# Kernel optimization log

Hardware: AMD Instinct MI355X
Metric: run time of the kernel (lower is better)

## Reference

```python
import jax, jax.numpy as jnp
import numpy as np

D_MODEL = 1024
NUM_HEADS = 16
D_K = D_MODEL // NUM_HEADS
TEMPERATURE = 1.0
EPS = 1e-6


def setup_inputs() -> dict:
    key = jax.random.key(0)
    ks = jax.random.split(key, 8)
    B, S, D, H = 2, 2048, D_MODEL, NUM_HEADS
    sc = 1.0 / np.sqrt(D)
    x = jax.random.normal(ks[0], (B, S, D), dtype=jnp.float32)
    Wq = jax.random.normal(ks[1], (D, D), dtype=jnp.float32) * sc
    Wk = jax.random.normal(ks[2], (D, D), dtype=jnp.float32) * sc
    Wv = jax.random.normal(ks[3], (D, D), dtype=jnp.float32) * sc
    Wo = jax.random.normal(ks[4], (D, D), dtype=jnp.float32) * sc
    bo = jnp.zeros((D,), dtype=jnp.float32)
    phase_scale = jnp.ones((H,), dtype=jnp.float32)
    # orthogonal init for entanglement matrix
    q, _ = np.linalg.qr(np.random.default_rng(0).normal(size=(H, H)))
    ent = jnp.asarray(q, dtype=jnp.float32)
    gamma = jnp.ones((D,), dtype=jnp.float32)
    beta = jnp.zeros((D,), dtype=jnp.float32)
    return {"x": x, "Wq": Wq, "Wk": Wk, "Wv": Wv, "Wo": Wo, "bo": bo,
            "phase_scale": phase_scale, "ent": ent, "gamma": gamma, "beta": beta}


def reference(x, Wq, Wk, Wv, Wo, bo, phase_scale, ent, gamma, beta):
    B, S, D = x.shape
    H, dk = NUM_HEADS, D_K
    # projections -> [B, H, S, dk]
    Q = (x @ Wq).reshape(B, S, H, dk).transpose(0, 2, 1, 3)
    K = (x @ Wk).reshape(B, S, H, dk).transpose(0, 2, 1, 3)
    V = (x @ Wv).reshape(B, S, H, dk).transpose(0, 2, 1, 3)
    # per-head QK^T, scaled, phase-modulated
    scores = jnp.einsum('bhqd,bhkd->bhqk', Q, K)
    inv = 1.0 / (float(np.sqrt(dk)) * TEMPERATURE)
    s = scores * (inv * phase_scale)[None, :, None, None]
    # real part of quantum phase: cos(s) + 0.1*cos(2s)  (imag part of V is zero,
    # so head_output = attended_real; the 0.1*attended_imag term vanishes)
    w = jnp.cos(s) + 0.1 * jnp.cos(2.0 * s)
    w = jax.nn.softmax(w, axis=-1)
    att = jnp.einsum('bhqk,bhkd->bhqd', w, V).transpose(0, 2, 1, 3)  # [B,S,H,dk]
    # faithful reproduction of tf.einsum('bsnd,hm->bsmd', ...): sums over n AND h
    att = jnp.einsum('bsnd,hm->bsmd', att, ent)
    out = att.reshape(B, S, D) @ Wo + bo
    r = out + x
    mu = jnp.mean(r, axis=-1, keepdims=True)
    var = jnp.mean(jnp.square(r - mu), axis=-1, keepdims=True)
    return gamma * (r - mu) * jax.lax.rsqrt(var + EPS) + beta
```

## Files before the change

### kernel.cpp

```cpp
#include <hip/hip_runtime.h>
#include <cstdint>
#include <cstddef>

#define S_LEN 2048
#define DMODEL 1024
#define NHEADS 16
#define DKH 64
#define MROWS 4096
#define BH_CNT 32

typedef __bf16 bf16x8 __attribute__((ext_vector_type(8)));
typedef __bf16 bf16x2 __attribute__((ext_vector_type(2)));
typedef float f32x4 __attribute__((ext_vector_type(4)));
typedef unsigned int u32;
typedef unsigned short u16;

__device__ __forceinline__ u16 f2bfu(float f) {
  u32 u = __float_as_uint(f);
  return (u16)((u + 0x7FFFu + ((u >> 16) & 1u)) >> 16);
}

__device__ __forceinline__ u32 pk_bf16(float a, float b) {
  bf16x2 v;
  v[0] = (__bf16)a;
  v[1] = (__bf16)b;
  return __builtin_bit_cast(u32, v);
}

__device__ __forceinline__ void gload16(void* lds, const void* g) {
  __builtin_amdgcn_global_load_lds(
      (const __attribute__((address_space(1))) void*)g,
      (__attribute__((address_space(3))) void*)lds, 16, 0, 0);
}

__global__ __launch_bounds__(256) void prep_xb_k(const float* __restrict__ x,
                                                 u16* __restrict__ xb) {
  int i = (blockIdx.x * 256 + threadIdx.x) * 4;
  float4 v = *(const float4*)(x + i);
  *(uint2*)(xb + i) = make_uint2(pk_bf16(v.x, v.y), pk_bf16(v.z, v.w));
}

__global__ __launch_bounds__(256) void prep_w_k(const float* __restrict__ Wq,
    const float* __restrict__ Wk, const float* __restrict__ Wv,
    const float* __restrict__ ps, u16* __restrict__ Wb) {
  __shared__ float tile[32][33];
  int sel = blockIdx.z;
  const float* W = sel == 0 ? Wq : (sel == 1 ? Wk : Wv);
  int k0 = blockIdx.x * 32, c0 = blockIdx.y * 32;
  int tx = threadIdx.x, ty = threadIdx.y;
#pragma unroll
  for (int i = 0; i < 4; ++i)
    tile[ty + i * 8][tx] = W[(size_t)(k0 + ty + i * 8) * DMODEL + c0 + tx];
  __syncthreads();
#pragma unroll
  for (int i = 0; i < 4; ++i) {
    int row = ty + i * 8;
    float v = tile[tx][row];
    if (sel == 1) v *= 0.125f * ps[(c0 + row) >> 6];
    Wb[(size_t)(sel * 1024 + c0 + row) * DMODEL + k0 + tx] = f2bfu(v);
  }
}

__global__ __launch_bounds__(256) void prep_woeff_k(const float* __restrict__ Wo,
    const float* __restrict__ ent, float* __restrict__ Woeff) {
  __shared__ float e[16];
  int t = threadIdx.x;
  if (t < 16) {
    float s = 0.f;
#pragma unroll
    for (int h = 0; h < 16; ++h) s += ent[h * 16 + t];
    e[t] = s;
  }
  __syncthreads();
  int gid = blockIdx.x * 256 + t;
  int d = gid >> 10, j = gid & 1023;
  float acc = 0.f;
#pragma unroll
  for (int m = 0; m < 16; ++m) acc += e[m] * Wo[(size_t)((m << 6) + d) * DMODEL + j];
  Woeff[(size_t)d * DMODEL + j] = acc;
}

__global__ __launch_bounds__(256) void gemm_qkv_k(const u16* __restrict__ xb,
    const u16* __restrict__ Wb, u16* __restrict__ Qb, u16* __restrict__ Kb,
    u16* __restrict__ Vt) {
  __shared__ __align__(16) u16 As[2][128 * 32];
  __shared__ __align__(16) u16 Bs[2][128 * 32];
  int tid = threadIdx.x;
  int lane = tid & 63, w = tid >> 6;
  int c = lane & 15, g = lane >> 4;
  int wr = w >> 1, wc = w & 1;
  int m0 = blockIdx.x * 128, n0 = blockIdx.y * 128;

  int cij0 = (w * 2) * 64 + lane, cij1 = (w * 2 + 1) * 64 + lane;
  int row0 = cij0 >> 2, kp0 = (cij0 & 3) ^ (row0 & 3);
  int row1 = cij1 >> 2, kp1 = (cij1 & 3) ^ (row1 & 3);
  const u16* a0p = xb + (size_t)(m0 + row0) * DMODEL + kp0 * 8;
  const u16* a1p = xb + (size_t)(m0 + row1) * DMODEL + kp1 * 8;
  const u16* b0p = Wb + (size_t)(n0 + row0) * DMODEL + kp0 * 8;
  const u16* b1p = Wb + (size_t)(n0 + row1) * DMODEL + kp1 * 8;

  f32x4 acc[4][4];
#pragma unroll
  for (int i = 0; i < 4; ++i)
#pragma unroll
    for (int j = 0; j < 4; ++j) acc[i][j] = (f32x4){0.f, 0.f, 0.f, 0.f};

  gload16(&As[0][(w * 2) * 512], a0p);
  gload16(&As[0][(w * 2 + 1) * 512], a1p);
  gload16(&Bs[0][(w * 2) * 512], b0p);
  gload16(&Bs[0][(w * 2 + 1) * 512], b1p);
  __syncthreads();

  int cur = 0;
  for (int kt = 0; kt < DMODEL; kt += 32) {
    if (kt + 32 < DMODEL) {
      int nx = cur ^ 1, ko = kt + 32;
      gload16(&As[nx][(w * 2) * 512], a0p + ko);
      gload16(&As[nx][(w * 2 + 1) * 512], a1p + ko);
      gload16(&Bs[nx][(w * 2) * 512], b0p + ko);
      gload16(&Bs[nx][(w * 2 + 1) * 512], b1p + ko);
    }
    const u16* Ac = As[cur];
    const u16* Bc = Bs[cur];
    bf16x8 af[4], bf[4];
#pragma unroll
    for (int i = 0; i < 4; ++i) {
      int ra = wr * 64 + i * 16 + c;
      af[i] = *(const bf16x8*)(Ac + ra * 32 + ((g ^ (ra & 3)) * 8));
      int rb = wc * 64 + i * 16 + c;
      bf[i] = *(const bf16x8*)(Bc + rb * 32 + ((g ^ (rb & 3)) * 8));
    }
#pragma unroll
    for (int i = 0; i < 4; ++i)
#pragma unroll
      for (int j = 0; j < 4; ++j)
        acc[i][j] = __builtin_amdgcn_mfma_f32_16x16x32_bf16(af[i], bf[j], acc[i][j], 0, 0, 0);
    __syncthreads();
    cur ^= 1;
  }

  int sel = n0 >> 10;
  int nb = n0 & 1023;
#pragma unroll
  for (int i = 0; i < 4; ++i) {
    int mbase = m0 + wr * 64 + i * 16 + 4 * g;
    int b = mbase >> 11, sr = mbase & 2047;
#pragma unroll
    for (int jf = 0; jf < 4; ++jf) {
      int ncol = nb + wc * 64 + jf * 16 + c;
      int h = ncol >> 6, d = ncol & 63;
      int bh = b * 16 + h;
      if (sel == 2) {
        *(uint2*)(Vt + ((size_t)bh * DKH + d) * S_LEN + sr) =
            make_uint2(pk_bf16(acc[i][jf][0], acc[i][jf][1]),
                       pk_bf16(acc[i][jf][2], acc[i][jf][3]));
      } else {
        u16* dst = (sel == 0 ? Qb : Kb);
#pragma unroll
        for (int j = 0; j < 4; ++j) {
          __bf16 hv = (__bf16)acc[i][jf][j];
          dst[((size_t)bh * S_LEN + sr + j) * DKH + d] = __builtin_bit_cast(u16, hv);
        }
      }
    }
  }
}

__global__ __launch_bounds__(256) void attn_k(const u16* __restrict__ Qb,
    const u16* __restrict__ Kb, const u16* __restrict__ Vt,
    float* __restrict__ attbuf) {
  __shared__ __align__(16) u16 Ks[2][64 * 64];
  __shared__ __align__(16) u16 Vs[2][64 * 64];
  __shared__ __align__(16) u32 Ps[4 * 16 * 32];
  int bh = blockIdx.y;
  int tid = threadIdx.x;
  int lane = tid & 63, w = tid >> 6;
  int c = lane & 15, g = lane >> 4;
  int q0 = blockIdx.x * 64 + w * 16;
  const u16* Kbase = Kb + (size_t)bh * S_LEN * DKH;
  const u16* Vbase = Vt + (size_t)bh * DKH * S_LEN;

  int cij0 = (w * 2) * 64 + lane, cij1 = (w * 2 + 1) * 64 + lane;
  int srow0 = cij0 >> 3, skp0 = (cij0 & 7) ^ (srow0 & 7);
  int srow1 = cij1 >> 3, skp1 = (cij1 & 7) ^ (srow1 & 7);
  const u16* k0p = Kbase + (size_t)srow0 * DKH + skp0 * 8;
  const u16* k1p = Kbase + (size_t)srow1 * DKH + skp1 * 8;
  const u16* v0p = Vbase + (size_t)srow0 * S_LEN + skp0 * 8;
  const u16* v1p = Vbase + (size_t)srow1 * S_LEN + skp1 * 8;

  gload16(&Ks[0][(w * 2) * 512], k0p);
  gload16(&Ks[0][(w * 2 + 1) * 512], k1p);
  gload16(&Vs[0][(w * 2) * 512], v0p);
  gload16(&Vs[0][(w * 2 + 1) * 512], v1p);

  bf16x8 qf0, qf1;
  {
    const u16* qp = Qb + ((size_t)bh * S_LEN + q0 + c) * DKH + g * 8;
    qf0 = *(const bf16x8*)qp;
    qf1 = *(const bf16x8*)(qp + 32);
  }
  f32x4 attT[4];
#pragma unroll
  for (int i = 0; i < 4; ++i) attT[i] = (f32x4){0.f, 0.f, 0.f, 0.f};
  float dacc0 = 0.f, dacc1 = 0.f;
  u32* Pw = Ps + w * 512;
  int wAddr[4];
#pragma unroll
  for (int fm = 0; fm < 4; ++fm) {
    int kr0 = fm * 16 + 4 * g;
    int ch = (kr0 >> 3) ^ (c & 7);
    wAddr[fm] = c * 32 + ch * 4 + ((kr0 & 7) >> 1);
  }
  const float L2E = 1.4426950408889634f;

  __syncthreads();
  int cur = 0;
  for (int kt = 0; kt < S_LEN; kt += 64) {
    if (kt + 64 < S_LEN) {
      int nx = cur ^ 1, ko = kt + 64;
      gload16(&Ks[nx][(w * 2) * 512], k0p + (size_t)ko * DKH);
      gload16(&Ks[nx][(w * 2 + 1) * 512], k1p + (size_t)ko * DKH);
      gload16(&Vs[nx][(w * 2) * 512], v0p + ko);
      gload16(&Vs[nx][(w * 2 + 1) * 512], v1p + ko);
    }
    const u16* Kc = Ks[cur];
    const u16* Vc = Vs[cur];
    f32x4 sT[4];
#pragma unroll
    for (int fm = 0; fm < 4; ++fm) {
      int row = fm * 16 + c;
      bf16x8 a0 = *(const bf16x8*)(Kc + row * 64 + ((g ^ (row & 7)) * 8));
      bf16x8 a1 = *(const bf16x8*)(Kc + row * 64 + (((4 + g) ^ (row & 7)) * 8));
      f32x4 z = (f32x4){0.f, 0.f, 0.f, 0.f};
      z = __builtin_amdgcn_mfma_f32_16x16x32_bf16(a0, qf0, z, 0, 0, 0);
      z = __builtin_amdgcn_mfma_f32_16x16x32_bf16(a1, qf1, z, 0, 0, 0);
      sT[fm] = z;
    }
#pragma unroll
    for (int fm = 0; fm < 4; ++fm) {
      float pv[4];
#pragma unroll
      for (int j = 0; j < 4; ++j) {
        float cv = __cosf(sT[fm][j]);
        float w2 = __fmaf_rn(cv, __fmaf_rn(0.2f * L2E, cv, L2E), -0.1f * L2E);
        pv[j] = __builtin_amdgcn_exp2f(w2);
      }
      dacc0 += pv[0] + pv[1];
      dacc1 += pv[2] + pv[3];
      *(uint2*)(Pw + wAddr[fm]) = make_uint2(pk_bf16(pv[0], pv[1]), pk_bf16(pv[2], pv[3]));
    }
#pragma unroll
    for (int bb = 0; bb < 2; ++bb) {
      bf16x8 pf = *(const bf16x8*)(Pw + c * 32 + (((4 * bb + g) ^ (c & 7)) * 4));
#pragma unroll
      for (int fd = 0; fd < 4; ++fd) {
        int row = fd * 16 + c;
        bf16x8 vf = *(const bf16x8*)(Vc + row * 64 + ((((4 * bb + g) ^ (row & 7))) * 8));
        attT[fd] = __builtin_amdgcn_mfma_f32_16x16x32_bf16(vf, pf, attT[fd], 0, 0, 0);
      }
    }
    __syncthreads();
    cur ^= 1;
  }
  float dacc = dacc0 + dacc1;
  dacc += __shfl_xor(dacc, 16, 64);
  dacc += __shfl_xor(dacc, 32, 64);
  float inv = 1.f / dacc;
  float* ob = attbuf + ((size_t)bh * S_LEN + q0 + c) * DKH;
#pragma unroll
  for (int fd = 0; fd < 4; ++fd)
#pragma unroll
    for (int j = 0; j < 4; ++j)
      ob[fd * 16 + 4 * g + j] = attT[fd][j] * inv;
}

__global__ __launch_bounds__(256) void fuse_out_ln_k(const float* __restrict__ attbuf,
    const float* __restrict__ Woeff, const float* __restrict__ bo,
    const float* __restrict__ x, const float* __restrict__ gamma,
    const float* __restrict__ beta, float* __restrict__ out) {
  __shared__ float red[8][256];
  __shared__ __align__(16) float a[8][64];
  __shared__ float sred[8][4][2];
  int t = threadIdx.x;
  int r0 = blockIdx.x * 8;
  int d = t & 63, hg = t >> 6;
#pragma unroll
  for (int rr = 0; rr < 8; ++rr) {
    int m = r0 + rr, b = m >> 11, sr = m & 2047;
    float pa = 0.f;
#pragma unroll
    for (int hh = 0; hh < 4; ++hh) {
      int h = hg * 4 + hh;
      pa += attbuf[(((size_t)(b * 16 + h)) * S_LEN + sr) * DKH + d];
    }
    red[rr][t] = pa;
  }
  __syncthreads();
#pragma unroll
  for (int e = 0; e < 2; ++e) {
    int idx = t + e * 256;
    int rr = idx >> 6, dd = idx & 63;
    a[rr][dd] = red[rr][dd] + red[rr][64 + dd] + red[rr][128 + dd] + red[rr][192 + dd];
  }
  __syncthreads();

  float o[8][4];
#pragma unroll
  for (int rr = 0; rr < 8; ++rr) { o[rr][0] = o[rr][1] = o[rr][2] = o[rr][3] = 0.f; }
  int c4 = t * 4;
  for (int dd = 0; dd < 64; dd += 4) {
    float4 wv0 = *(const float4*)(Woeff + (size_t)(dd + 0) * DMODEL + c4);
    float4 wv1 = *(const float4*)(Woeff + (size_t)(dd + 1) * DMODEL + c4);
    float4 wv2 = *(const float4*)(Woeff + (size_t)(dd + 2) * DMODEL + c4);
    float4 wv3 = *(const float4*)(Woeff + (size_t)(dd + 3) * DMODEL + c4);
#pragma unroll
    for (int rr = 0; rr < 8; ++rr) {
      float4 av = *(const float4*)&a[rr][dd];
      o[rr][0] += av.x * wv0.x + av.y * wv1.x + av.z * wv2.x + av.w * wv3.x;
      o[rr][1] += av.x * wv0.y + av.y * wv1.y + av.z * wv2.y + av.w * wv3.y;
      o[rr][2] += av.x * wv0.z + av.y * wv1.z + av.z * wv2.z + av.w * wv3.z;
      o[rr][3] += av.x * wv0.w + av.y * wv1.w + av.z * wv2.w + av.w * wv3.w;
    }
  }
  float4 bv = *(const float4*)(bo + c4);
  int w = t >> 6, lane = t & 63;
#pragma unroll
  for (int rr = 0; rr < 8; ++rr) {
    int m = r0 + rr;
    float4 xv = *(const float4*)(x + (size_t)m * DMODEL + c4);
    o[rr][0] += bv.x + xv.x;
    o[rr][1] += bv.y + xv.y;
    o[rr][2] += bv.z + xv.z;
    o[rr][3] += bv.w + xv.w;
    float s = o[rr][0] + o[rr][1] + o[rr][2] + o[rr][3];
    float q = o[rr][0] * o[rr][0] + o[rr][1] * o[rr][1] + o[rr][2] * o[rr][2] + o[rr][3] * o[rr][3];
#pragma unroll
    for (int mm = 1; mm < 64; mm <<= 1) {
      s += __shfl_xor(s, mm, 64);
      q += __shfl_xor(q, mm, 64);
    }
    if (lane == 0) { sred[rr][w][0] = s; sred[rr][w][1] = q; }
  }
  __syncthreads();
  float4 gv = *(const float4*)(gamma + c4);
  float4 bev = *(const float4*)(beta + c4);
#pragma unroll
  for (int rr = 0; rr < 8; ++rr) {
    float s = sred[rr][0][0] + sred[rr][1][0] + sred[rr][2][0] + sred[rr][3][0];
    float q = sred[rr][0][1] + sred[rr][1][1] + sred[rr][2][1] + sred[rr][3][1];
    float mu = s * (1.f / 1024.f);
    float var = q * (1.f / 1024.f) - mu * mu;
    float rs = rsqrtf(var + 1e-6f);
    int m = r0 + rr;
    float4 ov;
    ov.x = gv.x * (o[rr][0] - mu) * rs + bev.x;
    ov.y = gv.y * (o[rr][1] - mu) * rs + bev.y;
    ov.z = gv.z * (o[rr][2] - mu) * rs + bev.z;
    ov.w = gv.w * (o[rr][3] - mu) * rs + bev.w;
    *(float4*)(out + (size_t)m * DMODEL + c4) = ov;
  }
}

extern "C" void kernel_launch(void* const* d_in, const int* in_sizes, int n_in,
                              void* d_out, int out_size, void* d_ws, size_t ws_size,
                              hipStream_t stream) {
  const float* x = (const float*)d_in[0];
  const float* Wq = (const float*)d_in[1];
  const float* Wk = (const float*)d_in[2];
  const float* Wv = (const float*)d_in[3];
  const float* Wo = (const float*)d_in[4];
  const float* bo = (const float*)d_in[5];
  const float* ps = (const float*)d_in[6];
  const float* ent = (const float*)d_in[7];
  const float* gamma = (const float*)d_in[8];
  const float* beta = (const float*)d_in[9];
  float* out = (float*)d_out;

  char* ws = (char*)d_ws;
  size_t o = 0;
  u16* xb = (u16*)(ws + o);    o += (size_t)MROWS * DMODEL * 2;
  u16* Wb = (u16*)(ws + o);    o += (size_t)3072 * 1024 * 2;
  u16* Qb = (u16*)(ws + o);    o += (size_t)BH_CNT * S_LEN * DKH * 2;
  u16* Kb = (u16*)(ws + o);    o += (size_t)BH_CNT * S_LEN * DKH * 2;
  u16* Vt = (u16*)(ws + o);    o += (size_t)BH_CNT * S_LEN * DKH * 2;
  float* Woeff = (float*)(ws + o);  o += (size_t)DKH * DMODEL * 4;
  float* attbuf = (float*)(ws + o); o += (size_t)BH_CNT * S_LEN * DKH * 4;

  prep_xb_k<<<dim3(4096), dim3(256), 0, stream>>>(x, xb);
  prep_w_k<<<dim3(32, 32, 3), dim3(32, 8), 0, stream>>>(Wq, Wk, Wv, ps, Wb);
  prep_woeff_k<<<dim3(256), dim3(256), 0, stream>>>(Wo, ent, Woeff);
  gemm_qkv_k<<<dim3(32, 24), dim3(256), 0, stream>>>(xb, Wb, Qb, Kb, Vt);
  attn_k<<<dim3(32, 32), dim3(256), 0, stream>>>(Qb, Kb, Vt, attbuf);
  fuse_out_ln_k<<<dim3(512), dim3(256), 0, stream>>>(attbuf, Woeff, bo, x, gamma, beta, out);
}
```

Measured before the change: 141.3 us.

## Stage QKV epilogue through LDS, swizzle attention grid, use hardware cos

The QKV GEMM epilogue now writes accumulators into shared memory with an XOR swizzle, then emits coalesced 16-byte stores for Q, K and transposed V. The attention kernel uses a flattened, swizzled block index, a manually unrolled double-buffer loop with MFMA priority hints, and float4 output stores. The cosine now uses the raw hardware instruction, which takes its input in revolutions, so the K weight scale folds in 1/(2π). This skips the range-reduction overhead at some accuracy risk for large arguments.

After: 139.1 us. About the same (-1.5%).

```diff
diff --git a/kernel.cpp b/kernel.cpp
--- a/kernel.cpp
+++ b/kernel.cpp
@@ -56,7 +56,7 @@
   for (int i = 0; i < 4; ++i) {
     int row = ty + i * 8;
     float v = tile[tx][row];
-    if (sel == 1) v *= 0.125f * ps[(c0 + row) >> 6];
+    if (sel == 1) v *= 0.019894367886486918f * ps[(c0 + row) >> 6];
     Wb[(size_t)(sel * 1024 + c0 + row) * DMODEL + k0 + tx] = f2bfu(v);
   }
 }
@@ -83,8 +83,7 @@
 __global__ __launch_bounds__(256) void gemm_qkv_k(const u16* __restrict__ xb,
     const u16* __restrict__ Wb, u16* __restrict__ Qb, u16* __restrict__ Kb,
     u16* __restrict__ Vt) {
-  __shared__ __align__(16) u16 As[2][128 * 32];
-  __shared__ __align__(16) u16 Bs[2][128 * 32];
+  __shared__ __align__(16) u16 SMEM[2][2][128 * 32];
   int tid = threadIdx.x;
   int lane = tid & 63, w = tid >> 6;
   int c = lane & 15, g = lane >> 4;
@@ -105,23 +104,23 @@
 #pragma unroll
     for (int j = 0; j < 4; ++j) acc[i][j] = (f32x4){0.f, 0.f, 0.f, 0.f};
 
-  gload16(&As[0][(w * 2) * 512], a0p);
-  gload16(&As[0][(w * 2 + 1) * 512], a1p);
-  gload16(&Bs[0][(w * 2) * 512], b0p);
-  gload16(&Bs[0][(w * 2 + 1) * 512], b1p);
+  gload16(&SMEM[0][0][(w * 2) * 512], a0p);
+  gload16(&SMEM[0][0][(w * 2 + 1) * 512], a1p);
+  gload16(&SMEM[1][0][(w * 2) * 512], b0p);
+  gload16(&SMEM[1][0][(w * 2 + 1) * 512], b1p);
   __syncthreads();
 
   int cur = 0;
   for (int kt = 0; kt < DMODEL; kt += 32) {
     if (kt + 32 < DMODEL) {
       int nx = cur ^ 1, ko = kt + 32;
-      gload16(&As[nx][(w * 2) * 512], a0p + ko);
-      gload16(&As[nx][(w * 2 + 1) * 512], a1p + ko);
-      gload16(&Bs[nx][(w * 2) * 512], b0p + ko);
-      gload16(&Bs[nx][(w * 2 + 1) * 512], b1p + ko);
-    }
-    const u16* Ac = As[cur];
-    const u16* Bc = Bs[cur];
+      gload16(&SMEM[0][nx][(w * 2) * 512], a0p + ko);
+      gload16(&SMEM[0][nx][(w * 2 + 1) * 512], a1p + ko);
+      gload16(&SMEM[1][nx][(w * 2) * 512], b0p + ko);
+      gload16(&SMEM[1][nx][(w * 2 + 1) * 512], b1p + ko);
+    }
+    const u16* Ac = SMEM[0][cur];
+    const u16* Bc = SMEM[1][cur];
     bf16x8 af[4], bf[4];
 #pragma unroll
     for (int i = 0; i < 4; ++i) {
@@ -140,29 +139,50 @@
   }
 
   int sel = n0 >> 10;
-  int nb = n0 & 1023;
-#pragma unroll
-  for (int i = 0; i < 4; ++i) {
-    int mbase = m0 + wr * 64 + i * 16 + 4 * g;
-    int b = mbase >> 11, sr = mbase & 2047;
-#pragma unroll
-    for (int jf = 0; jf < 4; ++jf) {
-      int ncol = nb + wc * 64 + jf * 16 + c;
-      int h = ncol >> 6, d = ncol & 63;
-      int bh = b * 16 + h;
-      if (sel == 2) {
-        *(uint2*)(Vt + ((size_t)bh * DKH + d) * S_LEN + sr) =
-            make_uint2(pk_bf16(acc[i][jf][0], acc[i][jf][1]),
-                       pk_bf16(acc[i][jf][2], acc[i][jf][3]));
-      } else {
-        u16* dst = (sel == 0 ? Qb : Kb);
+  char* Ls = (char*)&SMEM[0][0][0];
+  if (sel == 2) {
+#pragma unroll
+    for (int i = 0; i < 4; ++i)
+#pragma unroll
+      for (int jf = 0; jf < 4; ++jf) {
+        int n = wc * 64 + jf * 16 + c;
+        int m = wr * 64 + i * 16 + 4 * g;
+        int byte = n * 256 + ((m * 2) ^ ((n & 7) << 4));
+        *(uint2*)(Ls + byte) = make_uint2(pk_bf16(acc[i][jf][0], acc[i][jf][1]),
+                                          pk_bf16(acc[i][jf][2], acc[i][jf][3]));
+      }
+  } else {
+#pragma unroll
+    for (int i = 0; i < 4; ++i)
+#pragma unroll
+      for (int jf = 0; jf < 4; ++jf) {
+        int n = wc * 64 + jf * 16 + c;
 #pragma unroll
         for (int j = 0; j < 4; ++j) {
+          int m = wr * 64 + i * 16 + 4 * g + j;
+          int byte = m * 256 + ((n * 2) ^ ((m & 7) << 4));
           __bf16 hv = (__bf16)acc[i][jf][j];
-          dst[((size_t)bh * S_LEN + sr + j) * DKH + d] = __builtin_bit_cast(u16, hv);
+          *(u16*)(Ls + byte) = __builtin_bit_cast(u16, hv);
         }
       }
-    }
+  }
+  __syncthreads();
+  int r = tid >> 1, half = tid & 1;
+  int h0 = (n0 & 1023) >> 6;
+  int b = m0 >> 11, sbase = m0 & 2047;
+  u16* dst;
+  if (sel == 2) {
+    int bh = b * 16 + h0 + (r >> 6), d = r & 63;
+    dst = Vt + ((size_t)bh * DKH + d) * S_LEN + sbase + half * 64;
+  } else {
+    u16* base = (sel == 0 ? Qb : Kb);
+    int bh = b * 16 + h0 + half;
+    dst = base + ((size_t)bh * S_LEN + sbase + r) * DKH;
+  }
+#pragma unroll
+  for (int kk = 0; kk < 8; ++kk) {
+    int byte = r * 256 + ((half * 128 + kk * 16) ^ ((r & 7) << 4));
+    *(uint4*)(dst + kk * 8) = *(const uint4*)(Ls + byte);
   }
 }
 
@@ -172,11 +192,13 @@
   __shared__ __align__(16) u16 Ks[2][64 * 64];
   __shared__ __align__(16) u16 Vs[2][64 * 64];
   __shared__ __align__(16) u32 Ps[4 * 16 * 32];
-  int bh = blockIdx.y;
+  int fid = blockIdx.x;
+  int swz = (fid & 7) * 128 + (fid >> 3);
+  int bh = swz >> 5, qblk = swz & 31;
   int tid = threadIdx.x;
   int lane = tid & 63, w = tid >> 6;
   int c = lane & 15, g = lane >> 4;
-  int q0 = blockIdx.x * 64 + w * 16;
+  int q0 = qblk * 64 + w * 16;
   const u16* Kbase = Kb + (size_t)bh * S_LEN * DKH;
   const u16* Vbase = Vt + (size_t)bh * DKH * S_LEN;
 
@@ -213,19 +235,9 @@
   }
   const float L2E = 1.4426950408889634f;
 
-  __syncthreads();
-  int cur = 0;
-  for (int kt = 0; kt < S_LEN; kt += 64) {
-    if (kt + 64 < S_LEN) {
-      int nx = cur ^ 1, ko = kt + 64;
-      gload16(&Ks[nx][(w * 2) * 512], k0p + (size_t)ko * DKH);
-      gload16(&Ks[nx][(w * 2 + 1) * 512], k1p + (size_t)ko * DKH);
-      gload16(&Vs[nx][(w * 2) * 512], v0p + ko);
-      gload16(&Vs[nx][(w * 2 + 1) * 512], v1p + ko);
-    }
-    const u16* Kc = Ks[cur];
-    const u16* Vc = Vs[cur];
+  auto compute = [&](const u16* Kc, const u16* Vc) {
     f32x4 sT[4];
+    __builtin_amdgcn_s_setprio(1);
 #pragma unroll
     for (int fm = 0; fm < 4; ++fm) {
       int row = fm * 16 + c;
@@ -236,12 +248,13 @@
       z = __builtin_amdgcn_mfma_f32_16x16x32_bf16(a1, qf1, z, 0, 0, 0);
       sT[fm] = z;
     }
+    __builtin_amdgcn_s_setprio(0);
 #pragma unroll
     for (int fm = 0; fm < 4; ++fm) {
       float pv[4];
 #pragma unroll
       for (int j = 0; j < 4; ++j) {
-        float cv = __cosf(sT[fm][j]);
+        float cv = __builtin_amdgcn_cosf(sT[fm][j]);
         float w2 = __fmaf_rn(cv, __fmaf_rn(0.2f * L2E, cv, L2E), -0.1f * L2E);
         pv[j] = __builtin_amdgcn_exp2f(w2);
       }
@@ -249,6 +262,7 @@
       dacc1 += pv[2] + pv[3];
       *(uint2*)(Pw + wAddr[fm]) = make_uint2(pk_bf16(pv[0], pv[1]), pk_bf16(pv[2], pv[3]));
     }
+    __builtin_amdgcn_s_setprio(1);
 #pragma unroll
     for (int bb = 0; bb < 2; ++bb) {
       bf16x8 pf = *(const bf16x8*)(Pw + c * 32 + (((4 * bb + g) ^ (c & 7)) * 4));
@@ -259,8 +273,31 @@
         attT[fd] = __builtin_amdgcn_mfma_f32_16x16x32_bf16(vf, pf, attT[fd], 0, 0, 0);
       }
     }
+    __builtin_amdgcn_s_setprio(0);
+  };
+
+  const u16* kc0 = k0p;
+  const u16* kc1 = k1p;
+  const u16* vc0 = v0p;
+  const u16* vc1 = v1p;
+  __syncthreads();
+  for (int kt = 0; kt < S_LEN; kt += 128) {
+    kc0 += 64 * DKH; kc1 += 64 * DKH; vc0 += 64; vc1 += 64;
+    gload16(&Ks[1][(w * 2) * 512], kc0);
+    gload16(&Ks[1][(w * 2 + 1) * 512], kc1);
+    gload16(&Vs[1][(w * 2) * 512], vc0);
+    gload16(&Vs[1][(w * 2 + 1) * 512], vc1);
+    compute(Ks[0], Vs[0]);
     __syncthreads();
-    cur ^= 1;
+    if (kt + 128 < S_LEN) {
+      kc0 += 64 * DKH; kc1 += 64 * DKH; vc0 += 64; vc1 += 64;
+      gload16(&Ks[0][(w * 2) * 512], kc0);
+      gload16(&Ks[0][(w * 2 + 1) * 512], kc1);
+      gload16(&Vs[0][(w * 2) * 512], vc0);
+      gload16(&Vs[0][(w * 2 + 1) * 512], vc1);
+    }
+    compute(Ks[1], Vs[1]);
+    __syncthreads();
   }
   float dacc = dacc0 + dacc1;
   dacc += __shfl_xor(dacc, 16, 64);
@@ -268,10 +305,14 @@
   float inv = 1.f / dacc;
   float* ob = attbuf + ((size_t)bh * S_LEN + q0 + c) * DKH;
 #pragma unroll
-  for (int fd = 0; fd < 4; ++fd)
-#pragma unroll
-    for (int j = 0; j < 4; ++j)
-      ob[fd * 16 + 4 * g + j] = attT[fd][j] * inv;
+  for (int fd = 0; fd < 4; ++fd) {
+    float4 ov;
+    ov.x = attT[fd][0] * inv;
+    ov.y = attT[fd][1] * inv;
+    ov.z = attT[fd][2] * inv;
+    ov.w = attT[fd][3] * inv;
+    *(float4*)(ob + fd * 16 + 4 * g) = ov;
+  }
 }
 
 __global__ __launch_bounds__(256) void fuse_out_ln_k(const float* __restrict__ attbuf,
@@ -390,6 +431,6 @@
   prep_w_k<<<dim3(32, 32, 3), dim3(32, 8), 0, stream>>>(Wq, Wk, Wv, ps, Wb);
   prep_woeff_k<<<dim3(256), dim3(256), 0, stream>>>(Wo, ent, Woeff);
   gemm_qkv_k<<<dim3(32, 24), dim3(256), 0, stream>>>(xb, Wb, Qb, Kb, Vt);
-  attn_k<<<dim3(32, 32), dim3(256), 0, stream>>>(Qb, Kb, Vt, attbuf);
+  attn_k<<<dim3(1024), dim3(256), 0, stream>>>(Qb, Kb, Vt, attbuf);
   fuse_out_ln_k<<<dim3(512), dim3(256), 0, stream>>>(attbuf, Woeff, bo, x, gamma, beta, out);
 }
```
